# Optimization experiments

Measured on AMD Instinct MI355X. Metric: run time of the kernel, lower is better.

The kernel has to match this reference:

```python
import jax, jax.numpy as jnp
import numpy as np


def _paste_masks(det_outs, ins_outs, H, W):
    # det_outs: [B,N,6] = (cx, cy, w, h, cls, score); ins_outs: [B,N,mh,mw]
    B, N, mh, mw = ins_outs.shape
    score = det_outs[..., -1]
    thr = jnp.where(jnp.max(score) > 50.0, 50.0, -100.0)
    valid = score >= thr  # [B,N]

    box = jnp.maximum(det_outs, 1.0)
    cx, cy, w, h = box[..., 0], box[..., 1], box[..., 2], box[..., 3]
    xmin = jnp.clip(jnp.ceil(cx - w / 2.0).astype(jnp.int32), 0, W)
    xmax = jnp.clip(jnp.ceil(cx + w / 2.0).astype(jnp.int32), 0, W)
    ymin = jnp.clip(jnp.ceil(cy - h / 2.0).astype(jnp.int32), 0, H)
    ymax = jnp.clip(jnp.ceil(cy + h / 2.0).astype(jnp.int32), 0, H)
    out_h = (ymax - ymin).astype(jnp.float32)
    out_w = (xmax - xmin).astype(jnp.float32)

    # tf.image.resize(align_corners=True): src = dst * (in-1)/(out-1) (0 if out<=1)
    sy = jnp.where(out_h > 1.0, (mh - 1) / jnp.maximum(out_h - 1.0, 1.0), 0.0)  # [B,N]
    sx = jnp.where(out_w > 1.0, (mw - 1) / jnp.maximum(out_w - 1.0, 1.0), 0.0)

    ys = jnp.arange(H, dtype=jnp.float32)
    xs = jnp.arange(W, dtype=jnp.float32)
    src_y = (ys[None, None, :] - ymin[..., None].astype(jnp.float32)) * sy[..., None]  # [B,N,H]
    src_x = (xs[None, None, :] - xmin[..., None].astype(jnp.float32)) * sx[..., None]  # [B,N,W]
    src_y = jnp.clip(src_y, 0.0, float(mh - 1))
    src_x = jnp.clip(src_x, 0.0, float(mw - 1))

    y0 = jnp.floor(src_y).astype(jnp.int32)
    y1 = jnp.minimum(y0 + 1, mh - 1)
    wy = src_y - y0.astype(jnp.float32)
    x0 = jnp.floor(src_x).astype(jnp.int32)
    x1 = jnp.minimum(x0 + 1, mw - 1)
    wx = src_x - x0.astype(jnp.float32)

    # bilinear: interpolate rows first ([B,N,H,mw]), then columns ([B,N,H,W])
    y0b = jnp.broadcast_to(y0[..., None], (B, N, H, mw))
    y1b = jnp.broadcast_to(y1[..., None], (B, N, H, mw))
    rows0 = jnp.take_along_axis(ins_outs, y0b, axis=2)
    rows1 = jnp.take_along_axis(ins_outs, y1b, axis=2)
    rows = rows0 * (1.0 - wy[..., None]) + rows1 * wy[..., None]  # [B,N,H,mw]

    x0b = jnp.broadcast_to(x0[:, :, None, :], (B, N, H, W))
    x1b = jnp.broadcast_to(x1[:, :, None, :], (B, N, H, W))
    v0 = jnp.take_along_axis(rows, x0b, axis=3)
    v1 = jnp.take_along_axis(rows, x1b, axis=3)
    vals = v0 * (1.0 - wx[:, :, None, :]) + v1 * wx[:, :, None, :]  # [B,N,H,W]

    # pad region: zeros outside [ymin,ymax) x [xmin,xmax); scatter only valid boxes
    inside = ((ys[None, None, :, None] >= ymin[..., None, None].astype(jnp.float32))
              & (ys[None, None, :, None] < ymax[..., None, None].astype(jnp.float32))
              & (xs[None, None, None, :] >= xmin[..., None, None].astype(jnp.float32))
              & (xs[None, None, None, :] < xmax[..., None, None].astype(jnp.float32)))
    keep = inside & valid[..., None, None]
    return jnp.where(keep, vals, 0.0)


def setup_inputs() -> dict:
    key = jax.random.key(0)
    B, N, H, W, MH, MW = 4, 64, 512, 512, 28, 28
    k = jax.random.split(key, 8)
    images = jax.random.normal(k[0], (B, H, W, 3), dtype=jnp.float32)
    cx = jax.random.uniform(k[1], (B, N), minval=0.0, maxval=float(W))
    cy = jax.random.uniform(k[2], (B, N), minval=0.0, maxval=float(H))
    bw = jax.random.uniform(k[3], (B, N), minval=20.0, maxval=200.0)
    bh = jax.random.uniform(k[4], (B, N), minval=20.0, maxval=200.0)
    cls = jax.random.uniform(k[5], (B, N), minval=0.0, maxval=10.0)
    score = jax.random.uniform(k[6], (B, N), minval=0.0, maxval=10.0)
    det_outs = jnp.stack([cx, cy, bw, bh, cls, score], axis=-1)
    ins_outs = jax.random.uniform(k[7], (B, N, MH, MW), dtype=jnp.float32)
    return {"images": images, "det_outs": det_outs, "ins_outs": ins_outs}


def reference(images, det_outs, ins_outs):
    H, W = images.shape[1], images.shape[2]
    return _paste_masks(det_outs, ins_outs, H, W)
```

## Files before the change

### kernel.cpp

```cpp
#include <hip/hip_runtime.h>

#define B_ 4
#define N_ 64
#define H_ 512
#define W_ 512
#define MH 28
#define MW 28

__global__ __launch_bounds__(256) void params_kernel(const float* __restrict__ det,
                                                     float* __restrict__ p) {
    __shared__ float red[256];
    int t = threadIdx.x;
    float sc = det[t * 6 + 5];
    red[t] = sc;
    __syncthreads();
    for (int s = 128; s > 0; s >>= 1) {
        if (t < s) red[t] = fmaxf(red[t], red[t + s]);
        __syncthreads();
    }
    float thr = (red[0] > 50.0f) ? 50.0f : -100.0f;

    float cx = fmaxf(det[t * 6 + 0], 1.0f);
    float cy = fmaxf(det[t * 6 + 1], 1.0f);
    float w  = fmaxf(det[t * 6 + 2], 1.0f);
    float h  = fmaxf(det[t * 6 + 3], 1.0f);
    int xmin = min(max((int)ceilf(cx - w * 0.5f), 0), W_);
    int xmax = min(max((int)ceilf(cx + w * 0.5f), 0), W_);
    int ymin = min(max((int)ceilf(cy - h * 0.5f), 0), H_);
    int ymax = min(max((int)ceilf(cy + h * 0.5f), 0), H_);
    float out_h = (float)(ymax - ymin);
    float out_w = (float)(xmax - xmin);
    float sy = (out_h > 1.0f) ? (float)(MH - 1) / fmaxf(out_h - 1.0f, 1.0f) : 0.0f;
    float sx = (out_w > 1.0f) ? (float)(MW - 1) / fmaxf(out_w - 1.0f, 1.0f) : 0.0f;

    float* o = p + t * 8;
    o[0] = (float)ymin;
    o[1] = (float)ymax;
    o[2] = (float)xmin;
    o[3] = (float)xmax;
    o[4] = sy;
    o[5] = sx;
    o[6] = (sc >= thr) ? 1.0f : 0.0f;
    o[7] = 0.0f;
}

__global__ __launch_bounds__(256) void paste_kernel(const float* __restrict__ ins,
                                                    const float* __restrict__ p,
                                                    float* __restrict__ out) {
    int bid   = blockIdx.x;
    int bn    = bid >> 8;
    int chunk = bid & 255;
    int t     = threadIdx.x;
    int y     = chunk * 2 + (t >> 7);
    int x0    = (t & 127) << 2;

    const float* q = p + bn * 8;
    float yminf = q[0], ymaxf = q[1], xminf = q[2], xmaxf = q[3];
    float sy = q[4], sx = q[5], valid = q[6];

    float4 r = make_float4(0.f, 0.f, 0.f, 0.f);
    float yf = (float)y;
    if (valid != 0.0f && yf >= yminf && yf < ymaxf) {
        float src_y = fminf(fmaxf((yf - yminf) * sy, 0.0f), (float)(MH - 1));
        float y0f = floorf(src_y);
        int   y0  = (int)y0f;
        int   y1  = min(y0 + 1, MH - 1);
        float wy  = src_y - y0f;
        const float* m  = ins + (size_t)bn * (MH * MW);
        const float* m0 = m + y0 * MW;
        const float* m1 = m + y1 * MW;
        float vals[4];
#pragma unroll
        for (int j = 0; j < 4; ++j) {
            float xf = (float)(x0 + j);
            float v  = 0.0f;
            if (xf >= xminf && xf < xmaxf) {
                float src_x = fminf(fmaxf((xf - xminf) * sx, 0.0f), (float)(MW - 1));
                float x0f = floorf(src_x);
                int   xi0 = (int)x0f;
                int   xi1 = min(xi0 + 1, MW - 1);
                float wx  = src_x - x0f;
                float a0 = m0[xi0], b0 = m1[xi0];
                float a1 = m0[xi1], b1 = m1[xi1];
                float r0 = a0 * (1.0f - wy) + b0 * wy;
                float r1 = a1 * (1.0f - wy) + b1 * wy;
                v = r0 * (1.0f - wx) + r1 * wx;
            }
            vals[j] = v;
        }
        r = make_float4(vals[0], vals[1], vals[2], vals[3]);
    }
    float4* optr = (float4*)(out + ((size_t)bn * H_ + y) * W_ + x0);
    *optr = r;
}

extern "C" void kernel_launch(void* const* d_in, const int* in_sizes, int n_in,
                              void* d_out, int out_size, void* d_ws, size_t ws_size,
                              hipStream_t stream) {
    const float* det = (const float*)d_in[1];
    const float* ins = (const float*)d_in[2];
    float* out = (float*)d_out;
    float* params = (float*)d_ws;

    params_kernel<<<1, 256, 0, stream>>>(det, params);
    paste_kernel<<<B_ * N_ * (H_ / 2), 256, 0, stream>>>(ins, params, out);
}
```

Measured before the change: 45.52 us.

## Fuse params into paste kernel with multi-row tiles and nontemporal stores

Removes the separate params kernel: every block redundantly computes the global score max with wave shuffles and derives its own box parameters. Each block now writes 16 rows instead of 2, so per-column interpolation indices and weights are computed once and reused across rows, and the grid shrinks eightfold. Output writes use nontemporal stores to avoid cache pollution on a write-only 256MB output. The cost is a redundant 256-element reduction per block and fewer blocks to hide latency.

Result: slower. 57.73 us (+26.8%).

```diff
diff --git a/kernel.cpp b/kernel.cpp
--- a/kernel.cpp
+++ b/kernel.cpp
@@ -6,24 +6,33 @@
 #define W_ 512
 #define MH 28
 #define MW 28
+#define TILE_ROWS 16
 
-__global__ __launch_bounds__(256) void params_kernel(const float* __restrict__ det,
-                                                     float* __restrict__ p) {
-    __shared__ float red[256];
-    int t = threadIdx.x;
-    float sc = det[t * 6 + 5];
-    red[t] = sc;
+typedef float f32x4 __attribute__((ext_vector_type(4)));
+
+__global__ __launch_bounds__(256) void fused_paste(const float* __restrict__ det,
+                                                   const float* __restrict__ ins,
+                                                   float* __restrict__ out) {
+    int bid  = blockIdx.x;
+    int bn   = bid >> 5;
+    int tile = bid & 31;
+    int t    = threadIdx.x;
+
+    float m = det[t * 6 + 5];
+#pragma unroll
+    for (int off = 1; off < 64; off <<= 1) m = fmaxf(m, __shfl_xor(m, off));
+    __shared__ float wmax[4];
+    if ((t & 63) == 0) wmax[t >> 6] = m;
     __syncthreads();
-    for (int s = 128; s > 0; s >>= 1) {
-        if (t < s) red[t] = fmaxf(red[t], red[t + s]);
-        __syncthreads();
-    }
-    float thr = (red[0] > 50.0f) ? 50.0f : -100.0f;
+    float gmax = fmaxf(fmaxf(wmax[0], wmax[1]), fmaxf(wmax[2], wmax[3]));
+    float thr  = (gmax > 50.0f) ? 50.0f : -100.0f;
 
-    float cx = fmaxf(det[t * 6 + 0], 1.0f);
-    float cy = fmaxf(det[t * 6 + 1], 1.0f);
-    float w  = fmaxf(det[t * 6 + 2], 1.0f);
-    float h  = fmaxf(det[t * 6 + 3], 1.0f);
+    const float* d6 = det + bn * 6;
+    float cx = fmaxf(d6[0], 1.0f);
+    float cy = fmaxf(d6[1], 1.0f);
+    float w  = fmaxf(d6[2], 1.0f);
+    float h  = fmaxf(d6[3], 1.0f);
+    float sc = d6[5];
     int xmin = min(max((int)ceilf(cx - w * 0.5f), 0), W_);
     int xmax = min(max((int)ceilf(cx + w * 0.5f), 0), W_);
     int ymin = min(max((int)ceilf(cy - h * 0.5f), 0), H_);
@@ -32,66 +41,55 @@
     float out_w = (float)(xmax - xmin);
     float sy = (out_h > 1.0f) ? (float)(MH - 1) / fmaxf(out_h - 1.0f, 1.0f) : 0.0f;
     float sx = (out_w > 1.0f) ? (float)(MW - 1) / fmaxf(out_w - 1.0f, 1.0f) : 0.0f;
+    bool valid = (sc >= thr);
 
-    float* o = p + t * 8;
-    o[0] = (float)ymin;
-    o[1] = (float)ymax;
-    o[2] = (float)xmin;
-    o[3] = (float)xmax;
-    o[4] = sy;
-    o[5] = sx;
-    o[6] = (sc >= thr) ? 1.0f : 0.0f;
-    o[7] = 0.0f;
-}
+    int x0   = (t & 127) << 2;
+    int lrow = t >> 7;
 
-__global__ __launch_bounds__(256) void paste_kernel(const float* __restrict__ ins,
-                                                    const float* __restrict__ p,
-                                                    float* __restrict__ out) {
-    int bid   = blockIdx.x;
-    int bn    = bid >> 8;
-    int chunk = bid & 255;
-    int t     = threadIdx.x;
-    int y     = chunk * 2 + (t >> 7);
-    int x0    = (t & 127) << 2;
+    int   xi0[4], xi1[4];
+    float wxv[4];
+    bool  okx[4];
+#pragma unroll
+    for (int j = 0; j < 4; ++j) {
+        int xp = x0 + j;
+        okx[j] = (xp >= xmin) && (xp < xmax);
+        float src_x = fminf(fmaxf(((float)xp - (float)xmin) * sx, 0.0f), (float)(MW - 1));
+        float xf = floorf(src_x);
+        xi0[j] = (int)xf;
+        xi1[j] = min(xi0[j] + 1, MW - 1);
+        wxv[j] = src_x - xf;
+    }
 
-    const float* q = p + bn * 8;
-    float yminf = q[0], ymaxf = q[1], xminf = q[2], xmaxf = q[3];
-    float sy = q[4], sx = q[5], valid = q[6];
+    const float* mk    = ins + (size_t)bn * (MH * MW);
+    float*       obase = out + (size_t)bn * (H_ * W_) + x0;
 
-    float4 r = make_float4(0.f, 0.f, 0.f, 0.f);
-    float yf = (float)y;
-    if (valid != 0.0f && yf >= yminf && yf < ymaxf) {
-        float src_y = fminf(fmaxf((yf - yminf) * sy, 0.0f), (float)(MH - 1));
-        float y0f = floorf(src_y);
-        int   y0  = (int)y0f;
-        int   y1  = min(y0 + 1, MH - 1);
-        float wy  = src_y - y0f;
-        const float* m  = ins + (size_t)bn * (MH * MW);
-        const float* m0 = m + y0 * MW;
-        const float* m1 = m + y1 * MW;
-        float vals[4];
 #pragma unroll
-        for (int j = 0; j < 4; ++j) {
-            float xf = (float)(x0 + j);
-            float v  = 0.0f;
-            if (xf >= xminf && xf < xmaxf) {
-                float src_x = fminf(fmaxf((xf - xminf) * sx, 0.0f), (float)(MW - 1));
-                float x0f = floorf(src_x);
-                int   xi0 = (int)x0f;
-                int   xi1 = min(xi0 + 1, MW - 1);
-                float wx  = src_x - x0f;
-                float a0 = m0[xi0], b0 = m1[xi0];
-                float a1 = m0[xi1], b1 = m1[xi1];
-                float r0 = a0 * (1.0f - wy) + b0 * wy;
-                float r1 = a1 * (1.0f - wy) + b1 * wy;
-                v = r0 * (1.0f - wx) + r1 * wx;
+    for (int p = 0; p < TILE_ROWS / 2; ++p) {
+        int y = tile * TILE_ROWS + p * 2 + lrow;
+        f32x4 r = (f32x4)0.0f;
+        if (valid && y >= ymin && y < ymax) {
+            float src_y = fminf(fmaxf(((float)y - (float)ymin) * sy, 0.0f), (float)(MH - 1));
+            float yf = floorf(src_y);
+            int   y0 = (int)yf;
+            int   y1 = min(y0 + 1, MH - 1);
+            float wy = src_y - yf;
+            const float* m0 = mk + y0 * MW;
+            const float* m1 = mk + y1 * MW;
+#pragma unroll
+            for (int j = 0; j < 4; ++j) {
+                float v = 0.0f;
+                if (okx[j]) {
+                    float a0 = m0[xi0[j]], b0 = m1[xi0[j]];
+                    float a1 = m0[xi1[j]], b1 = m1[xi1[j]];
+                    float r0 = a0 * (1.0f - wy) + b0 * wy;
+                    float r1 = a1 * (1.0f - wy) + b1 * wy;
+                    v = r0 * (1.0f - wxv[j]) + r1 * wxv[j];
+                }
+                r[j] = v;
             }
-            vals[j] = v;
         }
-        r = make_float4(vals[0], vals[1], vals[2], vals[3]);
+        __builtin_nontemporal_store(r, (f32x4*)(obase + (size_t)y * W_));
     }
-    float4* optr = (float4*)(out + ((size_t)bn * H_ + y) * W_ + x0);
-    *optr = r;
 }
 
 extern "C" void kernel_launch(void* const* d_in, const int* in_sizes, int n_in,
@@ -100,8 +98,6 @@
     const float* det = (const float*)d_in[1];
     const float* ins = (const float*)d_in[2];
     float* out = (float*)d_out;
-    float* params = (float*)d_ws;
 
-    params_kernel<<<1, 256, 0, stream>>>(det, params);
-    paste_kernel<<<B_ * N_ * (H_ / 2), 256, 0, stream>>>(ins, params, out);
+    fused_paste<<<B_ * N_ * (H_ / TILE_ROWS), 256, 0, stream>>>(det, ins, out);
 }
```
